# Kernel tuning notes

Measured on AMD Instinct MI355X. Metric: run time of the kernel, lower is better.

Reference implementation:

```python
import jax, jax.numpy as jnp
import numpy as np

D_MODEL = 768
N_HEADS = 12
D_HEAD = 64
BATCH = 4
SEQ = 2048
INIT_RANGE = 0.02
IGNORE = -1e5


def setup_inputs() -> dict:
    key = jax.random.key(0)
    ks = jax.random.split(key, 5)
    x = jax.random.normal(ks[0], (BATCH, SEQ, D_MODEL), dtype=jnp.float32)
    W_Q = jax.random.normal(ks[1], (N_HEADS, D_MODEL, D_HEAD), dtype=jnp.float32) * INIT_RANGE
    W_K = jax.random.normal(ks[2], (N_HEADS, D_MODEL, D_HEAD), dtype=jnp.float32) * INIT_RANGE
    W_V = jax.random.normal(ks[3], (N_HEADS, D_MODEL, D_HEAD), dtype=jnp.float32) * INIT_RANGE
    W_O = jax.random.normal(ks[4], (N_HEADS, D_HEAD, D_MODEL), dtype=jnp.float32) * INIT_RANGE
    b_Q = jnp.zeros((N_HEADS, D_HEAD), dtype=jnp.float32)
    b_K = jnp.zeros((N_HEADS, D_HEAD), dtype=jnp.float32)
    b_V = jnp.zeros((N_HEADS, D_HEAD), dtype=jnp.float32)
    b_O = jnp.zeros((D_MODEL,), dtype=jnp.float32)
    return {"normalized_resid_pre": x, "W_Q": W_Q, "W_K": W_K, "W_V": W_V,
            "W_O": W_O, "b_Q": b_Q, "b_K": b_K, "b_V": b_V, "b_O": b_O}


def reference(normalized_resid_pre, W_Q, W_K, W_V, W_O, b_Q, b_K, b_V, b_O):
    x = normalized_resid_pre  # [b, s, d_model]
    q = jnp.einsum('bsm,hmd->bshd', x, W_Q) + b_Q  # [b, s, h, d_head]
    k = jnp.einsum('bsm,hmd->bshd', x, W_K) + b_K
    v = jnp.einsum('bsm,hmd->bshd', x, W_V) + b_V
    scores = jnp.einsum('bqhd,bkhd->bhqk', q, k) / jnp.sqrt(jnp.float32(D_HEAD))
    seq = x.shape[1]
    causal = jnp.tril(jnp.ones((seq, seq), dtype=bool))  # True where allowed
    scores = jnp.where(causal, scores, jnp.float32(IGNORE))
    pattern = jax.nn.softmax(scores, axis=-1)  # [b, h, q, k]
    z = jnp.einsum('bhqk,bkhd->bqhd', pattern, v)
    attn_out = jnp.einsum('bqhd,hdm->bqm', z, W_O) + b_O
    return attn_out
```

## Files before the change

kernel.cpp:

```cpp
#include <hip/hip_runtime.h>
#include <math.h>

#define DEVI __device__ __forceinline__

typedef __bf16 bf16_t;
typedef bf16_t bf16x8 __attribute__((ext_vector_type(8)));
typedef float  f32x4  __attribute__((ext_vector_type(4)));

constexpr int NB   = 4;
constexpr int SEQL = 2048;
constexpr int NH   = 12;
constexpr int DHD  = 64;
constexpr int DMOD = 768;
constexpr int NT   = NB * SEQL;
constexpr int KD   = DMOD;


DEVI unsigned short f2bf(float f) {
  union { float f; unsigned u; } v; v.f = f;
  unsigned r = v.u + 0x7FFFu + ((v.u >> 16) & 1u);
  return (unsigned short)(r >> 16);
}

DEVI unsigned short cvt_bf16(float f) {
  bf16_t b = (bf16_t)f;
  return __builtin_bit_cast(unsigned short, b);
}

DEVI float exp2_raw(float x) {
  float r;
  asm("v_exp_f32 %0, %1" : "=v"(r) : "v"(x));
  return r;
}

DEVI void gload16(const unsigned short* src, unsigned short* dst) {
  auto g = (const __attribute__((address_space(1))) unsigned int*)(unsigned long long)src;
  auto l = (__attribute__((address_space(3))) unsigned int*)(unsigned int)(unsigned long long)(dst);
  __builtin_amdgcn_global_load_lds(g, l, 16, 0, 0);
}

__global__ void __launch_bounds__(256) prep_all(const float* __restrict__ x,
                                                const float* __restrict__ WQ,
                                                const float* __restrict__ WK,
                                                const float* __restrict__ WV,
                                                const float* __restrict__ WO,
                                                unsigned short* __restrict__ xb,
                                                unsigned short* __restrict__ Wt,
                                                unsigned short* __restrict__ Wo_t) {
  __shared__ float T[64][68];
  const int bid = blockIdx.x;
  const int t = threadIdx.x;
  if (bid < 3072) {
    size_t i = ((size_t)bid * 256 + t) * 8;
    float4 a = *(const float4*)(x + i);
    float4 b = *(const float4*)(x + i + 4);
    union { unsigned short u[8]; uint4 v; } pk;
    pk.u[0] = f2bf(a.x); pk.u[1] = f2bf(a.y); pk.u[2] = f2bf(a.z); pk.u[3] = f2bf(a.w);
    pk.u[4] = f2bf(b.x); pk.u[5] = f2bf(b.y); pk.u[6] = f2bf(b.z); pk.u[7] = f2bf(b.w);
    *(uint4*)(xb + i) = pk.v;
    return;
  }
  const int r0 = t >> 4, c4 = (t & 15) * 4;
  if (bid < 3504) {
    const int u = bid - 3072;
    const int mt = u % 12, hw = u / 12;
    const int which = hw / 12, h = hw % 12;
    const float* W = (which == 0) ? WQ : ((which == 1) ? WK : WV);
    const float* src = W + ((size_t)h * 768 + mt * 64) * 64;
#pragma unroll
    for (int rep = 0; rep < 4; ++rep) {
      int m = rep * 16 + r0;
      float4 v = *(const float4*)(src + m * 64 + c4);
      T[m][c4] = v.x; T[m][c4 + 1] = v.y; T[m][c4 + 2] = v.z; T[m][c4 + 3] = v.w;
    }
    __syncthreads();
    unsigned short* dst = Wt + ((size_t)which * 768 + h * 64) * 768 + mt * 64;
#pragma unroll
    for (int rep = 0; rep < 4; ++rep) {
      int d = rep * 16 + r0;
      union { unsigned short u[4]; uint2 v; } o;
#pragma unroll
      for (int j = 0; j < 4; ++j) o.u[j] = f2bf(T[c4 + j][d]);
      *(uint2*)(dst + (size_t)d * 768 + c4) = o.v;
    }
  } else {
    const int u = bid - 3504;
    const int m0 = (u % 12) * 64, hd0 = (u / 12) * 64;
#pragma unroll
    for (int rep = 0; rep < 4; ++rep) {
      int i = rep * 16 + r0;
      float4 v = *(const float4*)(WO + (size_t)(hd0 + i) * 768 + m0 + c4);
      T[i][c4] = v.x; T[i][c4 + 1] = v.y; T[i][c4 + 2] = v.z; T[i][c4 + 3] = v.w;
    }
    __syncthreads();
#pragma unroll
    for (int rep = 0; rep < 4; ++rep) {
      int m = rep * 16 + r0;
      union { unsigned short u[4]; uint2 v; } o;
#pragma unroll
      for (int j = 0; j < 4; ++j) o.u[j] = f2bf(T[c4 + j][m]);
      *(uint2*)(Wo_t + (size_t)(m0 + m) * 768 + hd0 + c4) = o.v;
    }
  }
}

__global__ void __launch_bounds__(256)
gemm_qkv(const unsigned short* __restrict__ A,
         const unsigned short* __restrict__ Bt,
         const float* __restrict__ bq, const float* __restrict__ bk,
         const float* __restrict__ bv,
         unsigned short* __restrict__ qo, unsigned short* __restrict__ ko,
         unsigned short* __restrict__ vo) {
  __shared__ __align__(16) unsigned short ldsA[2 * 8192];
  __shared__ __align__(16) unsigned short ldsB[8192];
  const int bm = blockIdx.x, bn = blockIdx.y;
  const int m0 = bm * 128, n0 = bn * 128;
  const int tid = threadIdx.x, w = tid >> 6, lane = tid & 63;
  const int g = lane >> 4, r16 = lane & 15;
  const int wm = w >> 1, wn = w & 1;

  const int ss = (lane & 7) ^ ((lane >> 3) & 7);
  const unsigned short* asrc = A  + (size_t)(m0 + (lane >> 3)) * KD + ss * 8;
  const unsigned short* bsrc = Bt + (size_t)(n0 + (lane >> 3)) * KD + ss * 8;

  auto stageA = [&](int buf, int kt) {
#pragma unroll
    for (int j = 0; j < 4; ++j) {
      int seg = w * 4 + j;
      gload16(asrc + (size_t)(seg * 8) * KD + kt * 64, ldsA + buf * 8192 + seg * 512);
    }
  };
  auto stageB = [&](int kt) {
#pragma unroll
    for (int j = 0; j < 4; ++j) {
      int seg = w * 4 + j;
      gload16(bsrc + (size_t)(seg * 8) * KD + kt * 64, ldsB + seg * 512);
    }
  };

  const int r7 = r16 & 7;
  const int aoff0 = r16 * 64 + ((g    ) ^ r7) * 8;
  const int aoff1 = r16 * 64 + ((g + 4) ^ r7) * 8;

  f32x4 acc[4][4];
  const f32x4 zero4 = {0.f, 0.f, 0.f, 0.f};
#pragma unroll
  for (int i = 0; i < 4; ++i)
#pragma unroll
    for (int j = 0; j < 4; ++j) acc[i][j] = zero4;

  constexpr int NKT = KD / 64;
  stageA(0, 0);
  stageB(0);
  int buf = 0;
  for (int kt = 0; kt < NKT; ++kt) {
    if (kt + 1 < NKT) {
      stageA(buf ^ 1, kt + 1);
      asm volatile("s_waitcnt vmcnt(4)" ::: "memory");
    } else {
      asm volatile("s_waitcnt vmcnt(0)" ::: "memory");
    }
    __builtin_amdgcn_s_barrier();
    const unsigned short* Ab = ldsA + buf * 8192 + wm * 4096;
    const unsigned short* Bb = ldsB + wn * 4096;
    bf16x8 af[2][4], bfr[2][4];
#pragma unroll
    for (int f = 0; f < 4; ++f) {
      af[0][f]  = *(const bf16x8*)&Ab[aoff0 + f * 1024];
      af[1][f]  = *(const bf16x8*)&Ab[aoff1 + f * 1024];
      bfr[0][f] = *(const bf16x8*)&Bb[aoff0 + f * 1024];
      bfr[1][f] = *(const bf16x8*)&Bb[aoff1 + f * 1024];
    }
#pragma unroll
    for (int kk = 0; kk < 2; ++kk)
#pragma unroll
      for (int fm = 0; fm < 4; ++fm)
#pragma unroll
        for (int fn = 0; fn < 4; ++fn)
          acc[fm][fn] = __builtin_amdgcn_mfma_f32_16x16x32_bf16(af[kk][fm], bfr[kk][fn],
                                                                acc[fm][fn], 0, 0, 0);
    asm volatile("s_waitcnt lgkmcnt(0)" ::: "memory");
    __builtin_amdgcn_s_barrier();
    if (kt + 1 < NKT) stageB(kt + 1);
    buf ^= 1;
  }

#pragma unroll
  for (int fm = 0; fm < 4; ++fm) {
#pragma unroll
    for (int fn = 0; fn < 4; ++fn) {
      const int col = n0 + wn * 64 + fn * 16 + r16;
      const int rbase = m0 + wm * 64 + fm * 16 + g * 4;
      const int which = (col >= 1536) ? 2 : ((col >= 768) ? 1 : 0);
      const int hd = col - which * 768;
      const int h = hd >> 6, d = hd & 63;
      const float bias = (which == 0 ? bq : which == 1 ? bk : bv)[hd];
      if (which == 2) {
        union { unsigned short u[4]; uint2 v; } o;
#pragma unroll
        for (int r = 0; r < 4; ++r) o.u[r] = cvt_bf16(acc[fm][fn][r] + bias);
        const int b = rbase >> 11, s = rbase & (SEQL - 1);
        *(uint2*)(vo + ((size_t)(b * NH + h) * DHD + d) * SEQL + s) = o.v;
      } else {
#pragma unroll
        for (int r = 0; r < 4; ++r) {
          int row = rbase + r;
          int b = row >> 11, s = row & (SEQL - 1);
          float v = acc[fm][fn][r] + bias;
          if (which == 0)
            qo[((size_t)(b * NH + h) * SEQL + s) * DHD + d] = cvt_bf16(v * 0.1803368801111f);
          else
            ko[((size_t)(b * NH + h) * SEQL + s) * DHD + d] = cvt_bf16(v);
        }
      }
    }
  }
}

__global__ void __launch_bounds__(256)
gemm_o(const unsigned short* __restrict__ A,
       const unsigned short* __restrict__ Bt,
       const float* __restrict__ bo, float* __restrict__ fout) {
  __shared__ __align__(16) unsigned short ldsA[2 * 4096];
  __shared__ __align__(16) unsigned short ldsB[8192];
  const int bm = blockIdx.x, bn = blockIdx.y;
  const int m0 = bm * 64, n0 = bn * 128;
  const int tid = threadIdx.x, w = tid >> 6, lane = tid & 63;
  const int g = lane >> 4, r16 = lane & 15;
  const int wm = w >> 1, wn = w & 1;

  const int ss = (lane & 7) ^ ((lane >> 3) & 7);
  const unsigned short* asrc = A  + (size_t)(m0 + (lane >> 3)) * KD + ss * 8;
  const unsigned short* bsrc = Bt + (size_t)(n0 + (lane >> 3)) * KD + ss * 8;

  auto stageA = [&](int buf, int kt) {
#pragma unroll
    for (int j = 0; j < 2; ++j) {
      int seg = w * 2 + j;
      gload16(asrc + (size_t)(seg * 8) * KD + kt * 64, ldsA + buf * 4096 + seg * 512);
    }
  };
  auto stageB = [&](int kt) {
#pragma unroll
    for (int j = 0; j < 4; ++j) {
      int seg = w * 4 + j;
      gload16(bsrc + (size_t)(seg * 8) * KD + kt * 64, ldsB + seg * 512);
    }
  };

  const int r7 = r16 & 7;
  const int aoff0 = r16 * 64 + ((g    ) ^ r7) * 8;
  const int aoff1 = r16 * 64 + ((g + 4) ^ r7) * 8;

  f32x4 acc[2][4];
  const f32x4 zero4 = {0.f, 0.f, 0.f, 0.f};
#pragma unroll
  for (int i = 0; i < 2; ++i)
#pragma unroll
    for (int j = 0; j < 4; ++j) acc[i][j] = zero4;

  constexpr int NKT = KD / 64;
  stageA(0, 0);
  stageB(0);
  int buf = 0;
  for (int kt = 0; kt < NKT; ++kt) {
    if (kt + 1 < NKT) {
      stageA(buf ^ 1, kt + 1);
      asm volatile("s_waitcnt vmcnt(2)" ::: "memory");
    } else {
      asm volatile("s_waitcnt vmcnt(0)" ::: "memory");
    }
    __builtin_amdgcn_s_barrier();
    const unsigned short* Ab = ldsA + buf * 4096 + wm * 2048;
    const unsigned short* Bb = ldsB + wn * 4096;
    bf16x8 af[2][2], bfr[2][4];
#pragma unroll
    for (int f = 0; f < 2; ++f) {
      af[0][f] = *(const bf16x8*)&Ab[aoff0 + f * 1024];
      af[1][f] = *(const bf16x8*)&Ab[aoff1 + f * 1024];
    }
#pragma unroll
    for (int f = 0; f < 4; ++f) {
      bfr[0][f] = *(const bf16x8*)&Bb[aoff0 + f * 1024];
      bfr[1][f] = *(const bf16x8*)&Bb[aoff1 + f * 1024];
    }
#pragma unroll
    for (int kk = 0; kk < 2; ++kk)
#pragma unroll
      for (int fm = 0; fm < 2; ++fm)
#pragma unroll
        for (int fn = 0; fn < 4; ++fn)
          acc[fm][fn] = __builtin_amdgcn_mfma_f32_16x16x32_bf16(af[kk][fm], bfr[kk][fn],
                                                                acc[fm][fn], 0, 0, 0);
    asm volatile("s_waitcnt lgkmcnt(0)" ::: "memory");
    __builtin_amdgcn_s_barrier();
    if (kt + 1 < NKT) stageB(kt + 1);
    buf ^= 1;
  }

#pragma unroll
  for (int fm = 0; fm < 2; ++fm) {
#pragma unroll
    for (int fn = 0; fn < 4; ++fn) {
      const int col = n0 + wn * 64 + fn * 16 + r16;
      const int rbase = m0 + wm * 32 + fm * 16 + g * 4;
      const float bias = bo[col];
#pragma unroll
      for (int r = 0; r < 4; ++r)
        fout[(size_t)(rbase + r) * DMOD + col] = acc[fm][fn][r] + bias;
    }
  }
}

__global__ void __launch_bounds__(256, 3)
attn_fwd(const unsigned short* __restrict__ qb,
         const unsigned short* __restrict__ kb,
         const unsigned short* __restrict__ vt,
         unsigned short* __restrict__ zb) {
  __shared__ __align__(16) unsigned short ldsK[2 * 4096];
  __shared__ __align__(16) unsigned short ldsV[2 * 4096];
  __shared__ __align__(16) unsigned short ldsP[4 * 1024];
  const int id = blockIdx.x;
  const int qp = id / 48, bh = id % 48;
  const int qtA = qp, qtB = 31 - qp;
  const int tid = threadIdx.x, w = tid >> 6, lane = tid & 63;
  const int g = lane >> 4, r16 = lane & 15;
  const int r7 = r16 & 7;

  const int sslot = (lane & 7) ^ (lane >> 3);
  const unsigned short* ksrc = kb + (size_t)bh * SEQL * DHD + (lane >> 3) * 64 + sslot * 8;
  const unsigned short* vsrc = vt + (size_t)bh * SEQL * DHD + (lane >> 3) * 2048 + sslot * 8;

  auto stage = [&](int buf, int kv0) {
#pragma unroll
    for (int j = 0; j < 2; ++j) {
      int seg = w * 2 + j;
      gload16(ksrc + kv0 * 64 + seg * 512, ldsK + buf * 4096 + seg * 512);
      gload16(vsrc + kv0 + seg * 16384,    ldsV + buf * 4096 + seg * 512);
    }
  };

  const int roff0 = r16 * 64 + ((g    ) ^ r7) * 8;
  const int roff1 = r16 * 64 + ((g + 4) ^ r7) * 8;
  char* const pwb = (char*)ldsP + w * 2048;
  int paddr[4];
#pragma unroll
  for (int fn = 0; fn < 4; ++fn)
    paddr[fn] = r16 * 128 + ((((fn * 2) + (g >> 1)) ^ r7) << 4) + ((g & 1) << 3);
  const int prd0 = r16 * 128 + (((g    ) ^ r7) << 4);
  const int prd1 = r16 * 128 + (((g + 4) ^ r7) << 4);
  const int thr = w * 16 + r16 - g * 4;

  bf16x8 qfA[2], qfB[2];
  {
    const unsigned short* qa = qb + ((size_t)bh * SEQL + qtA * 64 + w * 16 + r16) * DHD + g * 8;
    const unsigned short* qc = qb + ((size_t)bh * SEQL + qtB * 64 + w * 16 + r16) * DHD + g * 8;
    qfA[0] = *(const bf16x8*)qa; qfA[1] = *(const bf16x8*)(qa + 32);
    qfB[0] = *(const bf16x8*)qc; qfB[1] = *(const bf16x8*)(qc + 32);
  }

  float laccA = 0.f, laccB = 0.f;
  f32x4 zaccA[4], zaccB[4];
  const f32x4 zero4 = {0.f, 0.f, 0.f, 0.f};
#pragma unroll
  for (int r = 0; r < 4; ++r) { zaccA[r] = zero4; zaccB[r] = zero4; }

  auto tile_compute = [&](const bf16x8* qf, float& lacc, f32x4* zacc,
                          int buf, bool diag) {
    const unsigned short* Kb = ldsK + buf * 4096;
    const unsigned short* Vb = ldsV + buf * 4096;
    f32x4 sacc[4];
    __builtin_amdgcn_s_setprio(1);
#pragma unroll
    for (int fn = 0; fn < 4; ++fn) {
      bf16x8 kf = *(const bf16x8*)&Kb[roff0 + fn * 1024];
      sacc[fn] = __builtin_amdgcn_mfma_f32_16x16x32_bf16(kf, qf[0], zero4, 0, 0, 0);
    }
#pragma unroll
    for (int fn = 0; fn < 4; ++fn) {
      bf16x8 kf = *(const bf16x8*)&Kb[roff1 + fn * 1024];
      sacc[fn] = __builtin_amdgcn_mfma_f32_16x16x32_bf16(kf, qf[1], sacc[fn], 0, 0, 0);
    }
    __builtin_amdgcn_s_setprio(0);
    if (diag) {
#pragma unroll
      for (int fn = 0; fn < 4; ++fn)
#pragma unroll
        for (int r = 0; r < 4; ++r)
          if (fn * 16 + r > thr) sacc[fn][r] = -3.0e38f;
    }
#pragma unroll
    for (int fn = 0; fn < 4; ++fn) {
      float p0 = exp2_raw(sacc[fn][0]), p1 = exp2_raw(sacc[fn][1]);
      float p2 = exp2_raw(sacc[fn][2]), p3 = exp2_raw(sacc[fn][3]);
      lacc += (p0 + p1) + (p2 + p3);
      unsigned w0, w1;
      asm("v_cvt_pk_bf16_f32 %0, %1, %2" : "=v"(w0) : "v"(p0), "v"(p1));
      asm("v_cvt_pk_bf16_f32 %0, %1, %2" : "=v"(w1) : "v"(p2), "v"(p3));
      uint2 pk; pk.x = w0; pk.y = w1;
      *(uint2*)(pwb + paddr[fn]) = pk;
    }
    asm volatile("" ::: "memory");
    bf16x8 pf0 = *(const bf16x8*)(pwb + prd0);
    bf16x8 pf1 = *(const bf16x8*)(pwb + prd1);
    __builtin_amdgcn_s_setprio(1);
#pragma unroll
    for (int fn = 0; fn < 4; ++fn) {
      bf16x8 vf = *(const bf16x8*)&Vb[roff0 + fn * 1024];
      zacc[fn] = __builtin_amdgcn_mfma_f32_16x16x32_bf16(pf0, vf, zacc[fn], 0, 0, 0);
    }
#pragma unroll
    for (int fn = 0; fn < 4; ++fn) {
      bf16x8 vf = *(const bf16x8*)&Vb[roff1 + fn * 1024];
      zacc[fn] = __builtin_amdgcn_mfma_f32_16x16x32_bf16(pf1, vf, zacc[fn], 0, 0, 0);
    }
    __builtin_amdgcn_s_setprio(0);
  };

  stage(0, 0);
  int buf = 0;
  for (int kt = 0; kt <= qtA; ++kt) {
    __builtin_amdgcn_s_barrier();
    int nkv = (kt < qtA) ? (kt + 1) * 64 : 0;
    stage(buf ^ 1, nkv);
    asm volatile("s_waitcnt vmcnt(4)" ::: "memory");
    tile_compute(qfA, laccA, zaccA, buf, kt == qtA);
    buf ^= 1;
  }
  for (int kt = 0; kt <= qtB; ++kt) {
    __builtin_amdgcn_s_barrier();
    if (kt < qtB) {
      stage(buf ^ 1, (kt + 1) * 64);
      asm volatile("s_waitcnt vmcnt(4)" ::: "memory");
    } else {
      asm volatile("s_waitcnt vmcnt(0)" ::: "memory");
    }
    tile_compute(qfB, laccB, zaccB, buf, kt == qtB);
    buf ^= 1;
  }

  laccA += __shfl_xor(laccA, 16); laccA += __shfl_xor(laccA, 32);
  laccB += __shfl_xor(laccB, 16); laccB += __shfl_xor(laccB, 32);
  const float invA = 1.0f / laccA;
  const float invB = 1.0f / laccB;
  const int b = bh / NH, h = bh % NH;
#pragma unroll
  for (int r = 0; r < 4; ++r) {
    float iar = __shfl(invA, g * 4 + r);
    float ibr = __shfl(invB, g * 4 + r);
    int sA = qtA * 64 + w * 16 + g * 4 + r;
    int sB = qtB * 64 + w * 16 + g * 4 + r;
#pragma unroll
    for (int fn = 0; fn < 4; ++fn) {
      int d = fn * 16 + r16;
      zb[((size_t)(b * SEQL + sA)) * DMOD + h * DHD + d] = cvt_bf16(zaccA[fn][r] * iar);
      zb[((size_t)(b * SEQL + sB)) * DMOD + h * DHD + d] = cvt_bf16(zaccB[fn][r] * ibr);
    }
  }
}


extern "C" void kernel_launch(void* const* d_in, const int* in_sizes, int n_in,
                              void* d_out, int out_size, void* d_ws, size_t ws_size,
                              hipStream_t stream) {
  const float* x  = (const float*)d_in[0];
  const float* WQ = (const float*)d_in[1];
  const float* WK = (const float*)d_in[2];
  const float* WV = (const float*)d_in[3];
  const float* WO = (const float*)d_in[4];
  const float* bQ = (const float*)d_in[5];
  const float* bK = (const float*)d_in[6];
  const float* bV = (const float*)d_in[7];
  const float* bO = (const float*)d_in[8];
  float* out = (float*)d_out;

  constexpr size_t NE = (size_t)NT * DMOD;
  unsigned short* w0   = (unsigned short*)d_ws;
  unsigned short* Wqkv = w0;
  unsigned short* Wo   = Wqkv + (size_t)3 * 768 * 768;
  unsigned short* xb   = Wo + (size_t)768 * 768;
  unsigned short* qb   = xb + NE;
  unsigned short* kb   = qb + NE;
  unsigned short* vt   = kb + NE;
  unsigned short* zb   = xb;
  size_t need = (size_t)(vt + NE - w0) * sizeof(unsigned short);
  if (ws_size < need) return;

  prep_all<<<3648, 256, 0, stream>>>(x, WQ, WK, WV, WO, xb, Wqkv, Wo);
  gemm_qkv<<<dim3(64, 18), 256, 0, stream>>>(xb, Wqkv, bQ, bK, bV, qb, kb, vt);
  attn_fwd<<<768, 256, 0, stream>>>(qb, kb, vt, zb);
  gemm_o<<<dim3(128, 6), 256, 0, stream>>>(zb, Wo, bO, out);
}
```

Measured before the change: 106.1 us.

## Share K/V tile loads between paired query tiles in one KV loop

After: 106.0 us, median of 2. About the same (-0.0%).

```diff
diff --git a/kernel.cpp b/kernel.cpp
--- a/kernel.cpp
+++ b/kernel.cpp
@@ -319,7 +319,7 @@
          unsigned short* __restrict__ zb) {
   __shared__ __align__(16) unsigned short ldsK[2 * 4096];
   __shared__ __align__(16) unsigned short ldsV[2 * 4096];
-  __shared__ __align__(16) unsigned short ldsP[4 * 1024];
+  __shared__ __align__(16) unsigned short ldsP[2 * 4096];
   const int id = blockIdx.x;
   const int qp = id / 48, bh = id % 48;
   const int qtA = qp, qtB = 31 - qp;
@@ -342,7 +342,8 @@
 
   const int roff0 = r16 * 64 + ((g    ) ^ r7) * 8;
   const int roff1 = r16 * 64 + ((g + 4) ^ r7) * 8;
-  char* const pwb = (char*)ldsP + w * 2048;
+  char* const pwbA = (char*)ldsP + w * 2048;
+  char* const pwbB = (char*)ldsP + 8192 + w * 2048;
   int paddr[4];
 #pragma unroll
   for (int fn = 0; fn < 4; ++fn)
@@ -360,16 +361,13 @@
   }
 
   float laccA = 0.f, laccB = 0.f;
-  f32x4 zaccA[4], zaccB[4];
+  f32x4 zaccA[4], zaccB[4], saccA[4], saccB[4];
   const f32x4 zero4 = {0.f, 0.f, 0.f, 0.f};
 #pragma unroll
   for (int r = 0; r < 4; ++r) { zaccA[r] = zero4; zaccB[r] = zero4; }
 
-  auto tile_compute = [&](const bf16x8* qf, float& lacc, f32x4* zacc,
-                          int buf, bool diag) {
+  auto qk = [&](const bf16x8* qf, f32x4* sacc, int buf) {
     const unsigned short* Kb = ldsK + buf * 4096;
-    const unsigned short* Vb = ldsV + buf * 4096;
-    f32x4 sacc[4];
     __builtin_amdgcn_s_setprio(1);
 #pragma unroll
     for (int fn = 0; fn < 4; ++fn) {
@@ -382,6 +380,9 @@
       sacc[fn] = __builtin_amdgcn_mfma_f32_16x16x32_bf16(kf, qf[1], sacc[fn], 0, 0, 0);
     }
     __builtin_amdgcn_s_setprio(0);
+  };
+
+  auto sm = [&](f32x4* sacc, float& lacc, char* pwb, bool diag) {
     if (diag) {
 #pragma unroll
       for (int fn = 0; fn < 4; ++fn)
@@ -400,7 +401,10 @@
       uint2 pk; pk.x = w0; pk.y = w1;
       *(uint2*)(pwb + paddr[fn]) = pk;
     }
-    asm volatile("" ::: "memory");
+  };
+
+  auto pv = [&](char* pwb, f32x4* zacc, int buf) {
+    const unsigned short* Vb = ldsV + buf * 4096;
     bf16x8 pf0 = *(const bf16x8*)(pwb + prd0);
     bf16x8 pf1 = *(const bf16x8*)(pwb + prd1);
     __builtin_amdgcn_s_setprio(1);
@@ -418,24 +422,26 @@
   };
 
   stage(0, 0);
+  asm volatile("s_waitcnt vmcnt(0)" ::: "memory");
+  __builtin_amdgcn_s_barrier();
+
   int buf = 0;
-  for (int kt = 0; kt <= qtA; ++kt) {
-    __builtin_amdgcn_s_barrier();
-    int nkv = (kt < qtA) ? (kt + 1) * 64 : 0;
-    stage(buf ^ 1, nkv);
-    asm volatile("s_waitcnt vmcnt(4)" ::: "memory");
-    tile_compute(qfA, laccA, zaccA, buf, kt == qtA);
-    buf ^= 1;
-  }
   for (int kt = 0; kt <= qtB; ++kt) {
-    __builtin_amdgcn_s_barrier();
+    if (kt) __builtin_amdgcn_s_barrier();
     if (kt < qtB) {
       stage(buf ^ 1, (kt + 1) * 64);
-      asm volatile("s_waitcnt vmcnt(4)" ::: "memory");
+      if (kt) asm volatile("s_waitcnt vmcnt(4)" ::: "memory");
     } else {
       asm volatile("s_waitcnt vmcnt(0)" ::: "memory");
     }
-    tile_compute(qfB, laccB, zaccB, buf, kt == qtB);
+    const bool doA = (kt <= qtA);
+    qk(qfB, saccB, buf);
+    if (doA) qk(qfA, saccA, buf);
+    sm(saccB, laccB, pwbB, kt == qtB);
+    if (doA) sm(saccA, laccA, pwbA, kt == qtA);
+    asm volatile("" ::: "memory");
+    pv(pwbB, zaccB, buf);
+    if (doA) pv(pwbA, zaccA, buf);
     buf ^= 1;
   }
 
```
